# Kernel tuning notes

Measured on AMD Instinct MI355X. Metric: run time of the kernel, lower is better.

The kernel has to match this reference:

```python
import jax, jax.numpy as jnp
import numpy as np

K = 512
DIM = 256
BETA = 0.25


def setup_inputs() -> dict:
    key = jax.random.key(0)
    k1, k2 = jax.random.split(key)
    x = jax.random.normal(k1, (64, DIM, 32, 32), dtype=jnp.float32)
    lookup_table = jax.random.normal(k2, (K, DIM), dtype=jnp.float32)
    return {"x": x, "lookup_table": lookup_table}


def reference(x, lookup_table):
    b, d, h, w = x.shape
    # [b,d,h,w] -> [b*h*w, d]
    xf = jnp.transpose(x, (0, 2, 3, 1)).reshape(-1, d)
    # Squared Euclidean distances (argmin identical to torch.cdist argmin)
    d2 = (
        jnp.sum(xf * xf, axis=-1, keepdims=True)
        - 2.0 * (xf @ lookup_table.T)
        + jnp.sum(lookup_table * lookup_table, axis=-1)
    )  # [N, K]
    q = jnp.argmin(d2, axis=1)  # [N]
    x_e = lookup_table[q].reshape(b, h, w, d).transpose(0, 3, 1, 2)  # [b,d,h,w]
    q_x = q.reshape(b, h, w)
    codebook_loss = jnp.mean(jnp.square(jax.lax.stop_gradient(x) - x_e))
    commitment_loss = jnp.mean(jnp.square(x - jax.lax.stop_gradient(x_e)))
    loss = codebook_loss + BETA * commitment_loss
    return x_e, q_x, loss
```

## Files before the change

### kernel.cpp

```cpp
#include <hip/hip_runtime.h>

#define DIM     256
#define HW      1024
#define N_ROWS  65536
#define MARGIN  0.125f
#define MARGIN3 0.1875f

#define OUT_Q_OFF    16777216
#define OUT_LOSS_OFF 16842752

#define WS_DIST    512
#define WS_X2      2560
#define WS_CNTF_I  4608
#define WS_CNTP_I  4609
#define WS_LISTF_I 5120
#define WS_LISTP_I 21504
#define CAP_F      16384
#define CAP_P      32768
#define WS_LUTH_B  786432

#define VQ_LDS 132096

typedef _Float16 half8v __attribute__((ext_vector_type(8)));
typedef float floatx4 __attribute__((ext_vector_type(4)));

#define GLOAD_LDS16(gaddr, laddr) \
    __builtin_amdgcn_global_load_lds((const __attribute__((address_space(1))) unsigned int*)(gaddr), \
                                     (__attribute__((address_space(3))) unsigned int*)(laddr), 16, 0, 0)

__global__ void c2_kernel(const float* __restrict__ lut, float* __restrict__ ws) {
    if (threadIdx.x == 0) { ((int*)ws)[WS_CNTF_I] = 0; ((int*)ws)[WS_CNTP_I] = 0; }
    int t = threadIdx.x;
    for (int k = t; k < 512; k += 256) {
        const float4* row = (const float4*)(lut + (size_t)k * DIM);
        float s = 0.f;
        #pragma unroll 8
        for (int i = 0; i < DIM / 4; ++i) {
            float4 v = row[i];
            s += v.x * v.x + v.y * v.y + v.z * v.z + v.w * v.w;
        }
        ws[k] = s;
    }
}

__global__ void lutprep_kernel(const float* __restrict__ lut, float* __restrict__ ws) {
    int g = blockIdx.x * 256 + threadIdx.x;
    int lane = g & 63;
    int ctu  = (g >> 6) & 31;
    int dcg  = g >> 11;
    int code = ctu * 16 + (lane & 15);
    int d0   = dcg * 32 + (lane >> 4) * 8;
    const float* src = lut + (size_t)code * DIM + d0;
    half8v h;
    #pragma unroll
    for (int j = 0; j < 8; ++j) h[j] = (_Float16)src[j];
    char* dst = (char*)ws + WS_LUTH_B + (size_t)(dcg * 32 + ctu) * 1024 + lane * 16;
    *(half8v*)dst = h;
}

#define MERGE_TRIPLE(v1,i1,v2,i2,v3, w1,j1,w2,j2,w3)                          \
    {                                                                         \
        float a1,a2,a3,b1v,b2v; int a1i,a2i,b1i,b2i;                          \
        bool bf = (w1 < v1) || (w1 == v1 && j1 < i1);                         \
        if (bf) { a1=w1;a1i=j1;a2=w2;a2i=j2;a3=w3; b1v=v1;b1i=i1;b2v=v2;b2i=i2; } \
        else    { a1=v1;a1i=i1;a2=v2;a2i=i2;a3=v3; b1v=w1;b1i=j1;b2v=w2;b2i=j2; } \
        bool sa = (a2 < b1v) || (a2 == b1v && a2i < b1i);                     \
        v1 = a1; i1 = a1i;                                                    \
        if (sa) { v2 = a2; i2 = a2i; v3 = fminf(a3, b1v); }                   \
        else    { v2 = b1v; i2 = b1i; v3 = fminf(a2, b2v); }                  \
    }

__global__ __launch_bounds__(512, 1) void vq_kernel(const float* __restrict__ x,
                                                    const float* __restrict__ lut,
                                                    float* __restrict__ out,
                                                    float* __restrict__ ws) {
    extern __shared__ char smem[];
    int* qsh = (int*)(smem + 131072);
    const char* luth = (const char*)ws + WS_LUTH_B;

    const int tid  = threadIdx.x;
    const int blk  = blockIdx.x;
    const int wave = tid >> 6;
    const int lane = tid & 63;
    const int l15  = lane & 15;
    const int l4   = lane >> 4;

    const int n0w = blk * 256 + wave * 32;
    const int b   = n0w >> 10;
    const int hw0 = n0w & 1023;
    const float* xb = x + (size_t)b * (DIM * HW) + hw0;

    half8v a[2][8];
    float x2local = 0.f;
    #pragma unroll
    for (int t = 0; t < 2; ++t) {
        #pragma unroll
        for (int dc = 0; dc < 8; ++dc) {
            const float* src = xb + (size_t)(dc * 32 + l4 * 8) * HW + t * 16 + l15;
            half8v hh;
            #pragma unroll
            for (int j = 0; j < 8; ++j) {
                float v = src[(size_t)j * HW];
                x2local = fmaf(v, v, x2local);
                hh[j] = (_Float16)v;
            }
            a[t][dc] = hh;
        }
    }

    float v1[2][4], v2[2][4], v3[2][4]; int i1[2][4], i2[2][4];
    #pragma unroll
    for (int t = 0; t < 2; ++t)
        #pragma unroll
        for (int r = 0; r < 4; ++r) { v1[t][r]=3.4e38f; v2[t][r]=3.4e38f; v3[t][r]=3.4e38f; i1[t][r]=0; i2[t][r]=0; }

    for (int p = 0; p < 2; ++p) {
        __syncthreads();
        #pragma unroll
        for (int i = 0; i < 16; ++i) {
            int idx = i * 512 + tid;
            int ck  = idx >> 6;
            int sc  = (ck >> 4) * 32 + p * 16 + (ck & 15);
            GLOAD_LDS16(luth + (size_t)sc * 1024 + lane * 16, smem + ck * 1024);
        }
        __syncthreads();

        for (int cl = 0; cl < 16; ++cl) {
            half8v bh[8];
            #pragma unroll
            for (int dc = 0; dc < 8; ++dc)
                bh[dc] = *(const half8v*)(smem + (size_t)(dc * 16 + cl) * 1024 + lane * 16);
            floatx4 acc0 = (floatx4)0.f, acc1 = (floatx4)0.f;
            #pragma unroll
            for (int dc = 0; dc < 8; ++dc) {
                acc0 = __builtin_amdgcn_mfma_f32_16x16x32_f16(a[0][dc], bh[dc], acc0, 0, 0, 0);
                acc1 = __builtin_amdgcn_mfma_f32_16x16x32_f16(a[1][dc], bh[dc], acc1, 0, 0, 0);
            }
            const int code = (p * 16 + cl) * 16 + l15;
            const float c2v = ws[code];
            #pragma unroll
            for (int r = 0; r < 4; ++r) {
                float d0f = fmaf(-2.f, acc0[r], c2v);
                if (d0f < v1[0][r])      { v3[0][r]=v2[0][r]; v2[0][r]=v1[0][r]; i2[0][r]=i1[0][r]; v1[0][r]=d0f; i1[0][r]=code; }
                else if (d0f < v2[0][r]) { v3[0][r]=v2[0][r]; v2[0][r]=d0f; i2[0][r]=code; }
                else if (d0f < v3[0][r]) { v3[0][r]=d0f; }
                float d1f = fmaf(-2.f, acc1[r], c2v);
                if (d1f < v1[1][r])      { v3[1][r]=v2[1][r]; v2[1][r]=v1[1][r]; i2[1][r]=i1[1][r]; v1[1][r]=d1f; i1[1][r]=code; }
                else if (d1f < v2[1][r]) { v3[1][r]=v2[1][r]; v2[1][r]=d1f; i2[1][r]=code; }
                else if (d1f < v3[1][r]) { v3[1][r]=d1f; }
            }
        }
    }

    #pragma unroll
    for (int t = 0; t < 2; ++t) {
        #pragma unroll
        for (int r = 0; r < 4; ++r) {
            #pragma unroll
            for (int off = 1; off < 16; off <<= 1) {
                float w1 = __shfl_xor(v1[t][r], off, 64);
                int   j1 = __shfl_xor(i1[t][r], off, 64);
                float w2 = __shfl_xor(v2[t][r], off, 64);
                int   j2 = __shfl_xor(i2[t][r], off, 64);
                float w3 = __shfl_xor(v3[t][r], off, 64);
                MERGE_TRIPLE(v1[t][r], i1[t][r], v2[t][r], i2[t][r], v3[t][r], w1, j1, w2, j2, w3);
            }
        }
    }

    float dist_part = 0.f;
    if (l15 == 0) {
        #pragma unroll
        for (int t = 0; t < 2; ++t) {
            #pragma unroll
            for (int r = 0; r < 4; ++r) {
                int row = t * 16 + l4 * 4 + r;
                int n1 = i1[t][r];
                qsh[wave * 32 + row] = n1;
                out[OUT_Q_OFF + n0w + row] = (float)n1;
                float m1 = v1[t][r], m2 = v2[t][r], m3 = v3[t][r];
                if (m2 - m1 <= MARGIN) {
                    if (m3 - m1 > MARGIN3) {
                        int idx = atomicAdd((int*)ws + WS_CNTP_I, 1);
                        if (idx < CAP_P) {
                            ((int*)ws)[WS_LISTP_I + idx * 3 + 0] = n0w + row;
                            ((int*)ws)[WS_LISTP_I + idx * 3 + 1] = n1;
                            ((int*)ws)[WS_LISTP_I + idx * 3 + 2] = i2[t][r];
                        }
                    } else {
                        int idx = atomicAdd((int*)ws + WS_CNTF_I, 1);
                        if (idx < CAP_F) ((int*)ws)[WS_LISTF_I + idx] = n0w + row;
                    }
                }
                dist_part += m1;
            }
        }
    }
    float dv = dist_part;
    #pragma unroll
    for (int off = 32; off; off >>= 1) dv += __shfl_down(dv, off, 64);
    if (lane == 0) ws[WS_DIST + blk * 8 + wave] = dv;
    float xv = x2local;
    #pragma unroll
    for (int off = 32; off; off >>= 1) xv += __shfl_down(xv, off, 64);
    if (lane == 0) ws[WS_X2 + blk * 8 + wave] = xv;

    __syncthreads();

    {
        const int rl    = lane & 31;
        const int dhalf = lane >> 5;
        const int q     = qsh[wave * 32 + rl];
        const float4* lr = (const float4*)(lut + (size_t)q * DIM + dhalf * 128);
        float* ob = out + (size_t)b * (DIM * HW) + (size_t)(dhalf * 128) * HW + hw0 + rl;
        #pragma unroll 8
        for (int i = 0; i < 32; ++i) {
            float4 c = lr[i];
            ob[(size_t)(i * 4 + 0) * HW] = c.x;
            ob[(size_t)(i * 4 + 1) * HW] = c.y;
            ob[(size_t)(i * 4 + 2) * HW] = c.z;
            ob[(size_t)(i * 4 + 3) * HW] = c.w;
        }
    }
}

__global__ void recheck_kernel(const float* __restrict__ x, const float* __restrict__ lut,
                               float* __restrict__ out, const float* __restrict__ ws) {
    __shared__ float xrow[DIM];
    __shared__ float carow[DIM];
    __shared__ float cbrow[DIM];
    __shared__ float frv[256];
    __shared__ int   fri[256];
    __shared__ int   qq;
    const int tid = threadIdx.x;

    int cntp = ((const int*)ws)[WS_CNTP_I];
    if (cntp > CAP_P) cntp = CAP_P;
    const int* lp = (const int*)ws + WS_LISTP_I;
    for (int e = blockIdx.x; e < cntp; e += gridDim.x) {
        const int row = lp[e * 3 + 0];
        const int ia  = lp[e * 3 + 1];
        const int ib  = lp[e * 3 + 2];
        const int b = row >> 10, hw = row & 1023;
        xrow[tid]  = x[(size_t)b * (DIM * HW) + (size_t)tid * HW + hw];
        carow[tid] = lut[(size_t)ia * DIM + tid];
        cbrow[tid] = lut[(size_t)ib * DIM + tid];
        __syncthreads();
        if (tid == 0) {
            float dota = 0.f, dotb = 0.f;
            for (int d = 0; d < DIM; ++d) {
                dota = fmaf(xrow[d], carow[d], dota);
                dotb = fmaf(xrow[d], cbrow[d], dotb);
            }
            float da = fmaf(-2.f, dota, ws[ia]);
            float db = fmaf(-2.f, dotb, ws[ib]);
            int q;
            if (da < db) q = ia;
            else if (db < da) q = ib;
            else q = (ia < ib) ? ia : ib;
            qq = q;
            out[OUT_Q_OFF + row] = (float)q;
        }
        __syncthreads();
        const int q = qq;
        out[(size_t)b * (DIM * HW) + (size_t)tid * HW + hw] = lut[(size_t)q * DIM + tid];
        __syncthreads();
    }

    int cntf = ((const int*)ws)[WS_CNTF_I];
    if (cntf > CAP_F) cntf = CAP_F;
    const int* lf = (const int*)ws + WS_LISTF_I;
    for (int e = blockIdx.x; e < cntf; e += gridDim.x) {
        const int row = lf[e];
        const int b = row >> 10, hw = row & 1023;
        xrow[tid] = x[(size_t)b * (DIM * HW) + (size_t)tid * HW + hw];
        __syncthreads();
        float bv = 3.4e38f; int bi = 0;
        #pragma unroll
        for (int k2 = 0; k2 < 2; ++k2) {
            int k = tid + k2 * 256;
            const float* cr = lut + (size_t)k * DIM;
            float dot = 0.f;
            for (int d = 0; d < DIM; ++d) dot = fmaf(xrow[d], cr[d], dot);
            float dist = fmaf(-2.f, dot, ws[k]);
            if (dist < bv || (dist == bv && k < bi)) { bv = dist; bi = k; }
        }
        frv[tid] = bv; fri[tid] = bi;
        __syncthreads();
        for (int s = 128; s; s >>= 1) {
            if (tid < s) {
                float ov = frv[tid + s]; int oi = fri[tid + s];
                if (ov < frv[tid] || (ov == frv[tid] && oi < fri[tid])) {
                    frv[tid] = ov; fri[tid] = oi;
                }
            }
            __syncthreads();
        }
        const int q = fri[0];
        if (tid == 0) out[OUT_Q_OFF + row] = (float)q;
        out[(size_t)b * (DIM * HW) + (size_t)tid * HW + hw] = lut[(size_t)q * DIM + tid];
        __syncthreads();
    }
}

__global__ void loss_kernel(float* __restrict__ out, const float* __restrict__ ws) {
    __shared__ float wsum[4];
    int tid = threadIdx.x;
    float s = 0.f;
    for (int i = tid; i < 4096; i += 256) s += ws[WS_DIST + i];
    #pragma unroll
    for (int off = 32; off; off >>= 1) s += __shfl_down(s, off, 64);
    if ((tid & 63) == 0) wsum[tid >> 6] = s;
    __syncthreads();
    if (tid == 0) {
        float total = wsum[0] + wsum[1] + wsum[2] + wsum[3];
        out[OUT_LOSS_OFF] = total * (1.25f / 16777216.f);
    }
}

extern "C" void kernel_launch(void* const* d_in, const int* in_sizes, int n_in,
                              void* d_out, int out_size, void* d_ws, size_t ws_size,
                              hipStream_t stream) {
    const float* x   = (const float*)d_in[0];
    const float* lut = (const float*)d_in[1];
    float* out = (float*)d_out;
    float* ws  = (float*)d_ws;

    (void)hipFuncSetAttribute((const void*)vq_kernel,
                              hipFuncAttributeMaxDynamicSharedMemorySize, VQ_LDS);

    c2_kernel<<<1, 256, 0, stream>>>(lut, ws);
    lutprep_kernel<<<64, 256, 0, stream>>>(lut, ws);
    vq_kernel<<<256, 512, VQ_LDS, stream>>>(x, lut, out, ws);
    recheck_kernel<<<2048, 256, 0, stream>>>(x, lut, out, ws);
    loss_kernel<<<1, 256, 0, stream>>>(out, ws);
}
```

Measured before the change: 133.0 us.

## Stage x tile through LDS with float4 loads and vectorize x_e stores

```diff
diff --git a/kernel.cpp b/kernel.cpp
--- a/kernel.cpp
+++ b/kernel.cpp
@@ -85,28 +85,42 @@
     const int l15  = lane & 15;
     const int l4   = lane >> 4;
 
-    const int n0w = blk * 256 + wave * 32;
-    const int b   = n0w >> 10;
-    const int hw0 = n0w & 1023;
+    const int n0b = blk * 256;
+    const int b   = n0b >> 10;
+    const int hw0 = n0b & 1023;
+    const int n0w = n0b + wave * 32;
     const float* xb = x + (size_t)b * (DIM * HW) + hw0;
 
+    float x2local = 0.f;
+    #pragma unroll 8
+    for (int i = 0; i < 32; ++i) {
+        int gid = i * 512 + tid;
+        int d   = gid >> 6;
+        int r4  = gid & 63;
+        float4 v = *(const float4*)(xb + (size_t)d * HW + r4 * 4);
+        x2local = fmaf(v.x, v.x, x2local);
+        x2local = fmaf(v.y, v.y, x2local);
+        x2local = fmaf(v.z, v.z, x2local);
+        x2local = fmaf(v.w, v.w, x2local);
+        const int chunk = (r4 >> 3) * 16 + ((r4 >> 2) & 1) * 8 + (d >> 5);
+        const int lbase = ((d >> 3) & 3) * 16;
+        const int joff  = (d & 7) * 2;
+        char* cbp = smem + chunk * 1024;
+        const float* vf = (const float*)&v;
+        #pragma unroll
+        for (int rr = 0; rr < 4; ++rr) {
+            int row15 = 4 * (r4 & 3) + rr;
+            *(_Float16*)(cbp + (lbase + row15) * 16 + joff) = (_Float16)vf[rr];
+        }
+    }
+    __syncthreads();
+
     half8v a[2][8];
-    float x2local = 0.f;
-    #pragma unroll
-    for (int t = 0; t < 2; ++t) {
-        #pragma unroll
-        for (int dc = 0; dc < 8; ++dc) {
-            const float* src = xb + (size_t)(dc * 32 + l4 * 8) * HW + t * 16 + l15;
-            half8v hh;
-            #pragma unroll
-            for (int j = 0; j < 8; ++j) {
-                float v = src[(size_t)j * HW];
-                x2local = fmaf(v, v, x2local);
-                hh[j] = (_Float16)v;
-            }
-            a[t][dc] = hh;
-        }
-    }
+    #pragma unroll
+    for (int t = 0; t < 2; ++t)
+        #pragma unroll
+        for (int dc = 0; dc < 8; ++dc)
+            a[t][dc] = *(const half8v*)(smem + (size_t)(wave * 16 + t * 8 + dc) * 1024 + lane * 16);
 
     float v1[2][4], v2[2][4], v3[2][4]; int i1[2][4], i2[2][4];
     #pragma unroll
@@ -207,20 +221,17 @@
 
     __syncthreads();
 
-    {
-        const int rl    = lane & 31;
-        const int dhalf = lane >> 5;
-        const int q     = qsh[wave * 32 + rl];
-        const float4* lr = (const float4*)(lut + (size_t)q * DIM + dhalf * 128);
-        float* ob = out + (size_t)b * (DIM * HW) + (size_t)(dhalf * 128) * HW + hw0 + rl;
-        #pragma unroll 8
-        for (int i = 0; i < 32; ++i) {
-            float4 c = lr[i];
-            ob[(size_t)(i * 4 + 0) * HW] = c.x;
-            ob[(size_t)(i * 4 + 1) * HW] = c.y;
-            ob[(size_t)(i * 4 + 2) * HW] = c.z;
-            ob[(size_t)(i * 4 + 3) * HW] = c.w;
-        }
+    #pragma unroll 8
+    for (int i = 0; i < 32; ++i) {
+        int gid = i * 512 + tid;
+        int d   = gid >> 6;
+        int r4  = gid & 63;
+        float4 c;
+        float* cp = (float*)&c;
+        #pragma unroll
+        for (int rr = 0; rr < 4; ++rr)
+            cp[rr] = lut[(size_t)qsh[4 * r4 + rr] * DIM + d];
+        *(float4*)(out + (size_t)b * (DIM * HW) + (size_t)d * HW + hw0 + r4 * 4) = c;
     }
 }
 
```

After: 160.6 us. 1.21x slower.
